# Performance work log

Measured on AMD Instinct MI355X. Metric: run time of the kernel, lower is better.

The kernel has to match this reference:

```python
import jax, jax.numpy as jnp
import numpy as np

N_LAYERS = 10


def _rel_graph_conv(x, src, dst, etype, W_rel, W_loop, b):
    # x: [N, h]; W_rel: [R, h, h] (per-relation weight), DGL low_mem style:
    # project all nodes by all relations, then gather per edge by (etype, src).
    xr = jnp.einsum('ni,rio->rno', x, W_rel)          # [R, N, h]
    m = xr[etype, src]                                 # [E, h] per-edge messages
    agg = jax.ops.segment_sum(m, dst, num_segments=x.shape[0])  # sum aggregation
    # DGL RelGraphConv defaults: self_loop=True, bias=True, no activation
    return agg + x @ W_loop + b


def setup_inputs() -> dict:
    key = jax.random.key(0)
    ks = jax.random.split(key, 12)
    N, E, F, H, R = 100000, 600000, 64, 128, 8
    inp = {
        'feats': jax.random.normal(ks[0], (N, F), dtype=jnp.float32),
        'src': jax.random.randint(ks[1], (E,), 0, N, dtype=jnp.int32),
        'dst': jax.random.randint(ks[2], (E,), 0, N, dtype=jnp.int32),
        'etype': jax.random.randint(ks[3], (E,), 0, R, dtype=jnp.int32),
    }
    s = 0.05
    inp['W_in'] = jax.random.normal(ks[4], (F, H), dtype=jnp.float32) * s
    inp['b_in'] = jnp.zeros((H,), dtype=jnp.float32)
    # stacked params for 10 layer-dependent GCNConv layers
    inp['W_rel'] = jax.random.normal(ks[5], (N_LAYERS, R, H, H), dtype=jnp.float32) * s
    inp['W_loop'] = jax.random.normal(ks[6], (N_LAYERS, H, H), dtype=jnp.float32) * s
    inp['b_rel'] = jnp.zeros((N_LAYERS, H), dtype=jnp.float32)
    inp['W_u1'] = jax.random.normal(ks[7], (N_LAYERS, 2 * H, 2 * H), dtype=jnp.float32) * s  # Linear(h+h, 2h)
    inp['b_u1'] = jnp.zeros((N_LAYERS, 2 * H), dtype=jnp.float32)
    inp['W_u2'] = jax.random.normal(ks[8], (N_LAYERS, 3 * H, H), dtype=jnp.float32) * s      # Linear(h+2h, h)
    inp['b_u2'] = jnp.zeros((N_LAYERS, H), dtype=jnp.float32)
    return inp


def reference(feats, src, dst, etype, W_in, b_in, W_rel, W_loop, b_rel, W_u1, b_u1, W_u2, b_u2):
    act = jnp.tanh  # activation_dict['tanh']
    x = act(feats @ W_in + b_in)  # conv_input
    for l in range(N_LAYERS):
        msg = _rel_graph_conv(x, src, dst, etype, W_rel[l], W_loop[l], b_rel[l])
        mid = act(jnp.concatenate([x, msg], axis=1) @ W_u1[l] + b_u1[l])
        out = jnp.concatenate([x, mid], axis=1) @ W_u2[l] + b_u2[l]
        x = act(out)
    return x
```

## Files before the change

kernel.cpp:

```cpp
#include <hip/hip_runtime.h>
#include <cstddef>


#define HID 128
#define NREL 8
#define NL 10

typedef __attribute__((ext_vector_type(8))) __bf16 bf16x8;
typedef __attribute__((ext_vector_type(4))) float f32x4;

__device__ __forceinline__ float fast_tanh(float x) {
  float cx = fminf(fmaxf(x, -10.f), 10.f);
  float z = exp2f(cx * 2.8853900817779268f);
  return (z - 1.f) * __builtin_amdgcn_rcpf(z + 1.f);
}

__global__ __launch_bounds__(256) void k_transpose(const float* __restrict__ W,
                                                   __bf16* __restrict__ Wt,
                                                   int K, int Nc,
                                                   int inDiv, int inScale, int inOff,
                                                   int outDiv, int outScale, int outOff) {
  __shared__ float t[32][33];
  int z = blockIdx.z;
  int zi = (z / inDiv) * inScale + (z % inDiv) + inOff;
  int zo = (z / outDiv) * outScale + (z % outDiv) + outOff;
  const float* Wz = W + (size_t)zi * K * Nc;
  __bf16* Wtz = Wt + (size_t)zo * K * Nc;
  int n0 = blockIdx.x * 32, k0 = blockIdx.y * 32;
#pragma unroll
  for (int i = 0; i < 4; i++) {
    int k = k0 + threadIdx.y + i * 8;
    int n = n0 + threadIdx.x;
    t[threadIdx.y + i * 8][threadIdx.x] = Wz[(size_t)k * Nc + n];
  }
  __syncthreads();
#pragma unroll
  for (int i = 0; i < 4; i++) {
    int n = n0 + threadIdx.y + i * 8;
    int k = k0 + threadIdx.x;
    Wtz[(size_t)n * K + k] = (__bf16)t[threadIdx.x][threadIdx.y + i * 8];
  }
}

__global__ __launch_bounds__(256) void k_fold_wu1(const float* __restrict__ Wu1,
                                                  const float* __restrict__ Wloop,
                                                  __bf16* __restrict__ wt) {
  int l = blockIdx.y;
  int n0 = blockIdx.x * 32;
  const float* wu1 = Wu1 + (size_t)l * 256 * 256;
  const float* wl = Wloop + (size_t)l * 128 * 128;
  __bf16* wtl = wt + (size_t)l * 256 * 256;
  __shared__ float bot[128][33];
  for (int t = threadIdx.x; t < 128 * 32; t += 256) {
    int j = t >> 5, c = t & 31;
    bot[j][c] = wu1[(size_t)(128 + j) * 256 + n0 + c];
  }
  __syncthreads();
  int k = threadIdx.x & 127;
  int half = threadIdx.x >> 7;
  float acc[16];
#pragma unroll
  for (int c = 0; c < 16; c++) acc[c] = 0.f;
  for (int j = 0; j < 128; j++) {
    float w = wl[(size_t)k * 128 + j];
#pragma unroll
    for (int c = 0; c < 16; c++) acc[c] += w * bot[j][half * 16 + c];
  }
#pragma unroll
  for (int c = 0; c < 16; c++) {
    int n = n0 + half * 16 + c;
    wtl[(size_t)n * 256 + k] = (__bf16)(wu1[(size_t)k * 256 + n] + acc[c]);
  }
}

__global__ __launch_bounds__(256) void k_cvt(const float* __restrict__ x,
                                             __bf16* __restrict__ y, int n4) {
  int i = blockIdx.x * 256 + threadIdx.x;
  if (i < n4) {
    float4 f = ((const float4*)x)[i];
    __bf16 o[4] = {(__bf16)f.x, (__bf16)f.y, (__bf16)f.z, (__bf16)f.w};
    *(uint2*)(y + (size_t)i * 4) = *(uint2*)o;
  }
}

__global__ __launch_bounds__(256) void k_zero(int* __restrict__ p, int n) {
  for (int i = blockIdx.x * 256 + threadIdx.x; i < n; i += gridDim.x * 256) p[i] = 0;
}

__global__ __launch_bounds__(256) void k_hist_row(const int* __restrict__ dst,
                                                  int E, int* __restrict__ rowCnt) {
  int e = blockIdx.x * 256 + threadIdx.x;
  if (e < E) atomicAdd(&rowCnt[dst[e]], 1);
}

__global__ __launch_bounds__(256) void k_scan_part(const int* __restrict__ rowCnt,
                                                   int nb, int* __restrict__ thrPre,
                                                   int* __restrict__ blkSum) {
  __shared__ int sdata[256];
  int tid = threadIdx.x;
  int gtid = blockIdx.x * 256 + tid;
  int tot = gridDim.x * 256;
  int chunk = (nb + tot - 1) / tot;
  int lo = gtid * chunk, hi = min(nb, lo + chunk);
  int s = 0;
  for (int i = lo; i < hi; i++) s += rowCnt[i];
  sdata[tid] = s;
  __syncthreads();
#pragma unroll
  for (int off = 1; off < 256; off <<= 1) {
    int t = (tid >= off) ? sdata[tid - off] : 0;
    __syncthreads();
    sdata[tid] += t;
    __syncthreads();
  }
  thrPre[gtid] = sdata[tid] - s;
  if (tid == 255) blkSum[blockIdx.x] = sdata[255];
}

__global__ __launch_bounds__(256) void k_scan_mid(const int* __restrict__ blkSum,
                                                  int nblk, int nb,
                                                  int* __restrict__ blkOff,
                                                  int* __restrict__ rowStart) {
  __shared__ int part[256];
  int tid = threadIdx.x;
  part[tid] = (tid < nblk) ? blkSum[tid] : 0;
  __syncthreads();
  if (tid == 0) {
    int a = 0;
    for (int i = 0; i < nblk; i++) { int v = part[i]; part[i] = a; a += v; }
    rowStart[nb] = a;
  }
  __syncthreads();
  if (tid < nblk) blkOff[tid] = part[tid];
}

__global__ __launch_bounds__(256) void k_scan_fin(const int* __restrict__ rowCnt,
                                                  int nb,
                                                  const int* __restrict__ thrPre,
                                                  const int* __restrict__ blkOff,
                                                  int* __restrict__ rowStart,
                                                  int* __restrict__ rowCur) {
  int tid = threadIdx.x;
  int gtid = blockIdx.x * 256 + tid;
  int tot = gridDim.x * 256;
  int chunk = (nb + tot - 1) / tot;
  int lo = gtid * chunk, hi = min(nb, lo + chunk);
  int run = blkOff[blockIdx.x] + thrPre[gtid];
  for (int i = lo; i < hi; i++) {
    rowStart[i] = run;
    rowCur[i] = run;
    run += rowCnt[i];
  }
}

__global__ __launch_bounds__(256) void k_place_row(const int* __restrict__ et,
                                                   const int* __restrict__ src,
                                                   const int* __restrict__ dst,
                                                   int* __restrict__ rowCur,
                                                   int* __restrict__ epk, int E) {
  int e = blockIdx.x * 256 + threadIdx.x;
  if (e < E) {
    int p = atomicAdd(&rowCur[dst[e]], 1);
    epk[p] = src[e] | (et[e] << 17);
  }
}

__global__ __launch_bounds__(256) void seg_sum(
    const __bf16* __restrict__ Z, const int* __restrict__ rowStart,
    const int* __restrict__ epk, const float* __restrict__ b_rel_l,
    __bf16* __restrict__ msgb, int N, int relBase, int zW) {
  int t16 = threadIdx.x & 15;
  int d = blockIdx.x * 16 + (threadIdx.x >> 4);
  if (d >= N) return;

  float acc[8];
  if (b_rel_l) {
#pragma unroll
    for (int z = 0; z < 8; z++) acc[z] = b_rel_l[t16 * 8 + z];
  } else {
    bf16x8 mv = *(const bf16x8*)(msgb + (size_t)d * HID + t16 * 8);
#pragma unroll
    for (int z = 0; z < 8; z++) acc[z] = (float)mv[z];
  }

  const int lo = rowStart[d], hi = rowStart[d + 1];
  for (int e0 = lo; e0 < hi; e0 += 4) {
    bf16x8 v[4];
    int take[4];
#pragma unroll
    for (int u = 0; u < 4; u++) {
      int e = e0 + u;
      int in = e < hi;
      int p = epk[in ? e : lo];
      int rr = (p >> 17) - relBase;
      int slot = rr & 3;
      v[u] = *(const bf16x8*)(Z + (size_t)(p & 0x1FFFF) * zW + slot * HID + t16 * 8);
      take[u] = in && ((unsigned)rr < 4u);
    }
#pragma unroll
    for (int u = 0; u < 4; u++) {
      if (take[u]) {
#pragma unroll
        for (int z = 0; z < 8; z++) acc[z] += (float)v[u][z];
      }
    }
  }

  bf16x8 o;
#pragma unroll
  for (int z = 0; z < 8; z++) o[z] = (__bf16)acc[z];
  *(bf16x8*)(msgb + (size_t)d * HID + t16 * 8) = o;
}

template <int K, int K0, int MINW>
__global__ __launch_bounds__(512, MINW) void gemm_lds(
    const __bf16* __restrict__ A0, const __bf16* __restrict__ A1,
    const __bf16* __restrict__ Bt, const float* __restrict__ bias,
    __bf16* __restrict__ Cb, float* __restrict__ Cf,
    int M, int Nc, int act) {
  constexpr int NS = K / 32;
  constexpr int NS0 = K0 / 32;
  constexpr int K1 = (K - K0) > 0 ? (K - K0) : 1;
  __shared__ __bf16 As[2][256][32];
  __shared__ __bf16 Bs[2][128][32];

  const int tid = threadIdx.x;

  int colt, mrow;
  {
    const int gx = gridDim.x;
    const int nb = gx * gridDim.y;
    const int id = blockIdx.x + blockIdx.y * gx;
    const int q = nb >> 3, r = nb & 7;
    const int xcd = id & 7, i = id >> 3;
    const int wk = (xcd < r) ? (xcd * (q + 1) + i)
                             : (r * (q + 1) + (xcd - r) * q + i);
    colt = wk % gx;
    mrow = wk / gx;
  }
  const int m0 = mrow * 256;
  const int bn0 = colt * 128;

  const int w = tid >> 6;
  const int lane = tid & 63;

  const int cA0 = w * 128 + lane;
  const int rA0 = cA0 >> 2, sA0 = cA0 & 3;
  const int cA1 = cA0 + 64;
  const int rA1 = cA1 >> 2, sA1 = cA1 & 3;
  const int cB = w * 64 + lane;
  const int rB = cB >> 2, sB = cB & 3;

  auto stage_step = [&](int b, int ks) {
    {
      const __bf16* g = Bt + (size_t)(bn0 + rB) * K + ks * 32 + sB * 8;
      __builtin_amdgcn_global_load_lds(
          (const __attribute__((address_space(1))) void*)g,
          (__attribute__((address_space(3))) void*)(&Bs[b][0][0] + (size_t)w * 512),
          16, 0, 0);
    }
    if (ks < NS0) {
      const __bf16* g0 = A0 + (size_t)(m0 + rA0) * K0 + ks * 32 + sA0 * 8;
      __builtin_amdgcn_global_load_lds(
          (const __attribute__((address_space(1))) void*)g0,
          (__attribute__((address_space(3))) void*)(&As[b][0][0] + (size_t)(w * 2 + 0) * 512),
          16, 0, 0);
      const __bf16* g1 = A0 + (size_t)(m0 + rA1) * K0 + ks * 32 + sA1 * 8;
      __builtin_amdgcn_global_load_lds(
          (const __attribute__((address_space(1))) void*)g1,
          (__attribute__((address_space(3))) void*)(&As[b][0][0] + (size_t)(w * 2 + 1) * 512),
          16, 0, 0);
    } else {
      const __bf16* g0 = A1 + (size_t)(m0 + rA0) * K1 + (ks - NS0) * 32 + sA0 * 8;
      __builtin_amdgcn_global_load_lds(
          (const __attribute__((address_space(1))) void*)g0,
          (__attribute__((address_space(3))) void*)(&As[b][0][0] + (size_t)(w * 2 + 0) * 512),
          16, 0, 0);
      const __bf16* g1 = A1 + (size_t)(m0 + rA1) * K1 + (ks - NS0) * 32 + sA1 * 8;
      __builtin_amdgcn_global_load_lds(
          (const __attribute__((address_space(1))) void*)g1,
          (__attribute__((address_space(3))) void*)(&As[b][0][0] + (size_t)(w * 2 + 1) * 512),
          16, 0, 0);
    }
  };

  const int ml = lane & 15, q2 = lane >> 4;
  const int wr = (w >> 1) * 64;
  const int wc = (w & 1) * 64;

  f32x4 acc[4][4];
#pragma unroll
  for (int i = 0; i < 4; i++)
#pragma unroll
    for (int j = 0; j < 4; j++)
#pragma unroll
      for (int r = 0; r < 4; r++) acc[i][j][r] = 0.f;

  stage_step(0, 0);
  if (NS > 1) stage_step(1, 1);

#pragma unroll
  for (int ks = 0; ks < NS; ks++) {
    const int cur = ks & 1;
    if (ks + 1 < NS) asm volatile("s_waitcnt vmcnt(3)" ::: "memory");
    else             asm volatile("s_waitcnt vmcnt(0)" ::: "memory");
    asm volatile("s_barrier" ::: "memory");

    bf16x8 af[4], bfr[4];
#pragma unroll
    for (int i = 0; i < 4; i++)
      af[i] = *(const bf16x8*)(&As[cur][wr + i * 16 + ml][q2 * 8]);
#pragma unroll
    for (int j = 0; j < 4; j++)
      bfr[j] = *(const bf16x8*)(&Bs[cur][wc + j * 16 + ml][q2 * 8]);
#pragma unroll
    for (int i = 0; i < 4; i++)
#pragma unroll
      for (int j = 0; j < 4; j++)
        acc[i][j] = __builtin_amdgcn_mfma_f32_16x16x32_bf16(af[i], bfr[j],
                                                            acc[i][j], 0, 0, 0);

    asm volatile("s_barrier" ::: "memory");
    if (ks + 2 < NS) stage_step(cur, ks + 2);
  }

#pragma unroll
  for (int i = 0; i < 4; i++) {
#pragma unroll
    for (int r = 0; r < 4; r++) {
      int grow = m0 + wr + i * 16 + q2 * 4 + r;
      if (grow >= M) continue;
#pragma unroll
      for (int j = 0; j < 4; j++) {
        int col = bn0 + wc + j * 16 + ml;
        float v = acc[i][j][r];
        if (bias) v += bias[col];
        if (act) v = fast_tanh(v);
        if (Cb) Cb[(size_t)grow * Nc + col] = (__bf16)v;
        if (Cf) Cf[(size_t)grow * Nc + col] = v;
      }
    }
  }
}

extern "C" void kernel_launch(void* const* d_in, const int* in_sizes, int n_in,
                              void* d_out, int out_size, void* d_ws, size_t ws_size,
                              hipStream_t stream) {
  const float* feats  = (const float*)d_in[0];
  const int*   src    = (const int*)d_in[1];
  const int*   dst    = (const int*)d_in[2];
  const int*   etype  = (const int*)d_in[3];
  const float* W_in   = (const float*)d_in[4];
  const float* b_in   = (const float*)d_in[5];
  const float* W_rel  = (const float*)d_in[6];
  const float* W_loop = (const float*)d_in[7];
  const float* b_rel  = (const float*)d_in[8];
  const float* W_u1   = (const float*)d_in[9];
  const float* b_u1   = (const float*)d_in[10];
  const float* W_u2   = (const float*)d_in[11];
  const float* b_u2   = (const float*)d_in[12];

  const int E = in_sizes[1];
  const int N = in_sizes[0] / 64;
  const int TS = HID * HID;

  __bf16* xb0  = (__bf16*)d_ws;
  __bf16* xb1  = xb0 + (size_t)N * HID;
  __bf16* msgb = xb1 + (size_t)N * HID;
  __bf16* U    = msgb + (size_t)N * HID;
  __bf16* Z    = U;
  __bf16* mid  = U;
  __bf16* featsb = U;
  __bf16* wt_in = U + (size_t)N * 640;
  __bf16* wt_z0 = wt_in + 128 * 64;
  __bf16* wt_z1 = wt_z0 + (size_t)10 * 4 * TS;
  __bf16* wt_u1 = wt_z1 + (size_t)10 * 4 * TS;
  __bf16* wt_u2 = wt_u1 + (size_t)10 * 256 * 256;
  int* rowCnt   = (int*)(wt_u2 + (size_t)10 * 128 * 384);
  int* rowStart = rowCnt + N;
  int* rowCur   = rowStart + N + 1;
  int* epk      = rowCur + N;
  int* thrPre   = epk + E;
  int* blkSum   = thrPre + 256 * 256;
  int* blkOff   = blkSum + 256;

  k_transpose<<<dim3(4, 2, 1), dim3(32, 8), 0, stream>>>(W_in, wt_in, 64, 128,
                                                         1, 1, 0, 1, 1, 0);
  k_transpose<<<dim3(4, 4, 40), dim3(32, 8), 0, stream>>>(W_rel, wt_z0, 128, 128,
                                                          4, 8, 0, 4, 4, 0);
  k_transpose<<<dim3(4, 4, 40), dim3(32, 8), 0, stream>>>(W_rel, wt_z1, 128, 128,
                                                          4, 8, 4, 4, 4, 0);
  k_transpose<<<dim3(8, 8, 10), dim3(32, 8), 0, stream>>>(W_u1, wt_u1, 256, 256,
                                                          1, 1, 0, 1, 1, 0);
  k_fold_wu1<<<dim3(8, 10), dim3(256), 0, stream>>>(W_u1, W_loop, wt_u1);
  k_transpose<<<dim3(4, 12, 10), dim3(32, 8), 0, stream>>>(W_u2, wt_u2, 384, 128,
                                                           1, 1, 0, 1, 1, 0);
  k_cvt<<<(N * 64 / 4 + 255) / 256, 256, 0, stream>>>(feats, featsb, N * 64 / 4);

  k_zero<<<128, 256, 0, stream>>>(rowCnt, N);
  k_hist_row<<<(E + 255) / 256, 256, 0, stream>>>(dst, E, rowCnt);
  k_scan_part<<<256, 256, 0, stream>>>(rowCnt, N, thrPre, blkSum);
  k_scan_mid<<<1, 256, 0, stream>>>(blkSum, 256, N, blkOff, rowStart);
  k_scan_fin<<<256, 256, 0, stream>>>(rowCnt, N, thrPre, blkOff, rowStart, rowCur);
  k_place_row<<<(E + 255) / 256, 256, 0, stream>>>(etype, src, dst, rowCur, epk, E);

  const dim3 blk(512);
  const int gm = (N + 255) / 256;
  const dim3 gseg((N + 15) / 16);

  gemm_lds<64, 64, 2><<<dim3(1, gm), blk, 0, stream>>>(
      featsb, featsb, wt_in, b_in, xb0, nullptr, N, HID, 1);

  for (int l = 0; l < NL; l++) {
    const __bf16* xin = (l & 1) ? xb1 : xb0;
    __bf16* xout = (l & 1) ? xb0 : xb1;

    gemm_lds<128, 128, 2><<<dim3(4, gm), blk, 0, stream>>>(
        xin, xin, wt_z0 + (size_t)l * 4 * TS, nullptr, Z, nullptr, N, 512, 0);
    seg_sum<<<gseg, dim3(256), 0, stream>>>(Z, rowStart, epk,
                                            b_rel + (size_t)l * HID,
                                            msgb, N, 0, 512);
    gemm_lds<128, 128, 2><<<dim3(4, gm), blk, 0, stream>>>(
        xin, xin, wt_z1 + (size_t)l * 4 * TS, nullptr, Z, nullptr, N, 512, 0);
    seg_sum<<<gseg, dim3(256), 0, stream>>>(Z, rowStart, epk, nullptr,
                                            msgb, N, 4, 512);

    gemm_lds<256, 128, 2><<<dim3(2, gm), blk, 0, stream>>>(
        xin, msgb, wt_u1 + (size_t)l * 256 * 256, b_u1 + (size_t)l * 256,
        mid, nullptr, N, 256, 1);

    gemm_lds<384, 128, 2><<<dim3(1, gm), blk, 0, stream>>>(
        xin, mid, wt_u2 + (size_t)l * HID * 384, b_u2 + (size_t)l * HID,
        (l == NL - 1) ? nullptr : xout,
        (l == NL - 1) ? (float*)d_out : nullptr,
        N, HID, 1);
  }
}
```

Measured before the change: 2.379 ms.

## Compute relation projections only for (relation, src) pairs used by edges

Builds per-relation flags and compacted index lists of source nodes that actually appear with each relation, then runs a gathered GEMM that projects only those rows into a compacted Z buffer. Edge records now store the compacted Z row instead of src/etype, and seg_sum reads from the compact layout. With about 600k edges over 800k (relation, node) pairs, roughly half the projection GEMM work is skipped. In exchange it adds one-time preprocessing kernels and gathered A-row loads, and the GEMM epilogue writes scalar bf16 values.

```diff
diff --git a/kernel.cpp b/kernel.cpp
--- a/kernel.cpp
+++ b/kernel.cpp
@@ -93,7 +93,26 @@
   if (e < E) atomicAdd(&rowCnt[dst[e]], 1);
 }
 
-__global__ __launch_bounds__(256) void k_scan_part(const int* __restrict__ rowCnt,
+__global__ __launch_bounds__(256) void k_flag(const int* __restrict__ et,
+                                              const int* __restrict__ src,
+                                              int E, int N,
+                                              int* __restrict__ F0,
+                                              int* __restrict__ F1) {
+  int e = blockIdx.x * 256 + threadIdx.x;
+  if (e < E) {
+    int r = et[e];
+    (r < 4 ? F0 : F1)[(r & 3) * N + src[e]] = 1;
+  }
+}
+
+__global__ __launch_bounds__(256) void k_srcof(const int* __restrict__ F,
+                                               const int* __restrict__ P,
+                                               int n, int N, int* __restrict__ srcOf) {
+  int i = blockIdx.x * 256 + threadIdx.x;
+  if (i < n && F[i]) srcOf[P[i]] = i % N;
+}
+
+__global__ __launch_bounds__(256) void k_scan_part(const int* __restrict__ cntArr,
                                                    int nb, int* __restrict__ thrPre,
                                                    int* __restrict__ blkSum) {
   __shared__ int sdata[256];
@@ -103,7 +122,7 @@
   int chunk = (nb + tot - 1) / tot;
   int lo = gtid * chunk, hi = min(nb, lo + chunk);
   int s = 0;
-  for (int i = lo; i < hi; i++) s += rowCnt[i];
+  for (int i = lo; i < hi; i++) s += cntArr[i];
   sdata[tid] = s;
   __syncthreads();
 #pragma unroll
@@ -120,7 +139,7 @@
 __global__ __launch_bounds__(256) void k_scan_mid(const int* __restrict__ blkSum,
                                                   int nblk, int nb,
                                                   int* __restrict__ blkOff,
-                                                  int* __restrict__ rowStart) {
+                                                  int* __restrict__ pre) {
   __shared__ int part[256];
   int tid = threadIdx.x;
   part[tid] = (tid < nblk) ? blkSum[tid] : 0;
@@ -128,18 +147,18 @@
   if (tid == 0) {
     int a = 0;
     for (int i = 0; i < nblk; i++) { int v = part[i]; part[i] = a; a += v; }
-    rowStart[nb] = a;
+    pre[nb] = a;
   }
   __syncthreads();
   if (tid < nblk) blkOff[tid] = part[tid];
 }
 
-__global__ __launch_bounds__(256) void k_scan_fin(const int* __restrict__ rowCnt,
+__global__ __launch_bounds__(256) void k_scan_fin(const int* __restrict__ cntArr,
                                                   int nb,
                                                   const int* __restrict__ thrPre,
                                                   const int* __restrict__ blkOff,
-                                                  int* __restrict__ rowStart,
-                                                  int* __restrict__ rowCur) {
+                                                  int* __restrict__ pre,
+                                                  int* __restrict__ cur) {
   int tid = threadIdx.x;
   int gtid = blockIdx.x * 256 + tid;
   int tot = gridDim.x * 256;
@@ -147,28 +166,34 @@
   int lo = gtid * chunk, hi = min(nb, lo + chunk);
   int run = blkOff[blockIdx.x] + thrPre[gtid];
   for (int i = lo; i < hi; i++) {
-    rowStart[i] = run;
-    rowCur[i] = run;
-    run += rowCnt[i];
+    pre[i] = run;
+    if (cur) cur[i] = run;
+    run += cntArr[i];
   }
 }
 
 __global__ __launch_bounds__(256) void k_place_row(const int* __restrict__ et,
                                                    const int* __restrict__ src,
                                                    const int* __restrict__ dst,
+                                                   const int* __restrict__ P0,
+                                                   const int* __restrict__ P1,
                                                    int* __restrict__ rowCur,
-                                                   int* __restrict__ epk, int E) {
+                                                   int* __restrict__ epk, int E, int N) {
   int e = blockIdx.x * 256 + threadIdx.x;
   if (e < E) {
     int p = atomicAdd(&rowCur[dst[e]], 1);
-    epk[p] = src[e] | (et[e] << 17);
+    int r = et[e];
+    int half = r >> 2;
+    const int* P = half ? P1 : P0;
+    int zrow = P[(r & 3) * N + src[e]];
+    epk[p] = zrow | (half << 19);
   }
 }
 
 __global__ __launch_bounds__(256) void seg_sum(
-    const __bf16* __restrict__ Z, const int* __restrict__ rowStart,
+    const __bf16* __restrict__ Zc, const int* __restrict__ rowStart,
     const int* __restrict__ epk, const float* __restrict__ b_rel_l,
-    __bf16* __restrict__ msgb, int N, int relBase, int zW) {
+    __bf16* __restrict__ msgb, int N, int half) {
   int t16 = threadIdx.x & 15;
   int d = blockIdx.x * 16 + (threadIdx.x >> 4);
   if (d >= N) return;
@@ -192,10 +217,9 @@
       int e = e0 + u;
       int in = e < hi;
       int p = epk[in ? e : lo];
-      int rr = (p >> 17) - relBase;
-      int slot = rr & 3;
-      v[u] = *(const bf16x8*)(Z + (size_t)(p & 0x1FFFF) * zW + slot * HID + t16 * 8);
-      take[u] = in && ((unsigned)rr < 4u);
+      int zrow = p & 0x7FFFF;
+      v[u] = *(const bf16x8*)(Zc + (size_t)zrow * HID + t16 * 8);
+      take[u] = in && ((p >> 19) == half);
     }
 #pragma unroll
     for (int u = 0; u < 4; u++) {
@@ -210,6 +234,118 @@
 #pragma unroll
   for (int z = 0; z < 8; z++) o[z] = (__bf16)acc[z];
   *(bf16x8*)(msgb + (size_t)d * HID + t16 * 8) = o;
+}
+
+__global__ __launch_bounds__(512, 2) void gemm_gather(
+    const __bf16* __restrict__ X, const __bf16* __restrict__ Wt4,
+    const int* __restrict__ srcOf, const int* __restrict__ Pf,
+    __bf16* __restrict__ Zc, int N) {
+  constexpr int K = 128, NS = 4;
+  __shared__ __bf16 As[2][256][32];
+  __shared__ __bf16 Bs[2][128][32];
+
+  const int tid = threadIdx.x;
+  int colt, mrow;
+  {
+    const int gx = gridDim.x;
+    const int nb = gx * gridDim.y;
+    const int id = blockIdx.x + blockIdx.y * gx;
+    const int q = nb >> 3, r8 = nb & 7;
+    const int xcd = id & 7, i = id >> 3;
+    const int wk = (xcd < r8) ? (xcd * (q + 1) + i)
+                              : (r8 * (q + 1) + (xcd - r8) * q + i);
+    colt = wk % gx;
+    mrow = wk / gx;
+  }
+  const int rel = colt;
+  const int base = Pf[rel * N];
+  const int nxt = Pf[(rel + 1) * N];
+  const int cnt = nxt - base;
+  const int m0 = mrow * 256;
+  if (m0 >= cnt) return;
+  const __bf16* Bt = Wt4 + (size_t)rel * K * 128;
+
+  const int w = tid >> 6, lane = tid & 63;
+  const int cA0 = w * 128 + lane;
+  const int rA0 = cA0 >> 2, sA0 = cA0 & 3;
+  const int cA1 = cA0 + 64;
+  const int rA1 = cA1 >> 2, sA1 = cA1 & 3;
+  const int cB = w * 64 + lane;
+  const int rB = cB >> 2, sB = cB & 3;
+
+  const int src0 = srcOf[min(base + m0 + rA0, nxt - 1)];
+  const int src1 = srcOf[min(base + m0 + rA1, nxt - 1)];
+  const __bf16* a0 = X + (size_t)src0 * K + sA0 * 8;
+  const __bf16* a1 = X + (size_t)src1 * K + sA1 * 8;
+
+  auto stage_step = [&](int b, int ks) {
+    const __bf16* g = Bt + (size_t)rB * K + ks * 32 + sB * 8;
+    __builtin_amdgcn_global_load_lds(
+        (const __attribute__((address_space(1))) void*)g,
+        (__attribute__((address_space(3))) void*)(&Bs[b][0][0] + (size_t)w * 512),
+        16, 0, 0);
+    __builtin_amdgcn_global_load_lds(
+        (const __attribute__((address_space(1))) void*)(a0 + ks * 32),
+        (__attribute__((address_space(3))) void*)(&As[b][0][0] + (size_t)(w * 2 + 0) * 512),
+        16, 0, 0);
+    __builtin_amdgcn_global_load_lds(
+        (const __attribute__((address_space(1))) void*)(a1 + ks * 32),
+        (__attribute__((address_space(3))) void*)(&As[b][0][0] + (size_t)(w * 2 + 1) * 512),
+        16, 0, 0);
+  };
+
+  const int ml = lane & 15, q2 = lane >> 4;
+  const int wr = (w >> 1) * 64, wc = (w & 1) * 64;
+
+  f32x4 acc[4][4];
+#pragma unroll
+  for (int i = 0; i < 4; i++)
+#pragma unroll
+    for (int j = 0; j < 4; j++)
+#pragma unroll
+      for (int r = 0; r < 4; r++) acc[i][j][r] = 0.f;
+
+  stage_step(0, 0);
+  stage_step(1, 1);
+
+#pragma unroll
+  for (int ks = 0; ks < NS; ks++) {
+    const int cur = ks & 1;
+    if (ks + 1 < NS) asm volatile("s_waitcnt vmcnt(3)" ::: "memory");
+    else             asm volatile("s_waitcnt vmcnt(0)" ::: "memory");
+    asm volatile("s_barrier" ::: "memory");
+
+    bf16x8 af[4], bfr[4];
+#pragma unroll
+    for (int i = 0; i < 4; i++)
+      af[i] = *(const bf16x8*)(&As[cur][wr + i * 16 + ml][q2 * 8]);
+#pragma unroll
+    for (int j = 0; j < 4; j++)
+      bfr[j] = *(const bf16x8*)(&Bs[cur][wc + j * 16 + ml][q2 * 8]);
+#pragma unroll
+    for (int i = 0; i < 4; i++)
+#pragma unroll
+      for (int j = 0; j < 4; j++)
+        acc[i][j] = __builtin_amdgcn_mfma_f32_16x16x32_bf16(af[i], bfr[j],
+                                                            acc[i][j], 0, 0, 0);
+
+    asm volatile("s_barrier" ::: "memory");
+    if (ks + 2 < NS) stage_step(cur, ks + 2);
+  }
+
+#pragma unroll
+  for (int i = 0; i < 4; i++) {
+#pragma unroll
+    for (int r = 0; r < 4; r++) {
+      int lrow = m0 + wr + i * 16 + q2 * 4 + r;
+      if (lrow >= cnt) continue;
+#pragma unroll
+      for (int j = 0; j < 4; j++) {
+        int col = wc + j * 16 + ml;
+        Zc[(size_t)(base + lrow) * HID + col] = (__bf16)acc[i][j][r];
+      }
+    }
+  }
 }
 
 template <int K, int K0, int MINW>
@@ -225,16 +361,15 @@
   __shared__ __bf16 Bs[2][128][32];
 
   const int tid = threadIdx.x;
-
   int colt, mrow;
   {
     const int gx = gridDim.x;
     const int nb = gx * gridDim.y;
     const int id = blockIdx.x + blockIdx.y * gx;
-    const int q = nb >> 3, r = nb & 7;
+    const int q = nb >> 3, r8 = nb & 7;
     const int xcd = id & 7, i = id >> 3;
-    const int wk = (xcd < r) ? (xcd * (q + 1) + i)
-                             : (r * (q + 1) + (xcd - r) * q + i);
+    const int wk = (xcd < r8) ? (xcd * (q + 1) + i)
+                              : (r8 * (q + 1) + (xcd - r8) * q + i);
     colt = wk % gx;
     mrow = wk / gx;
   }
@@ -383,6 +518,12 @@
   int* thrPre   = epk + E;
   int* blkSum   = thrPre + 256 * 256;
   int* blkOff   = blkSum + 256;
+  int* F0       = blkOff + 256;
+  int* F1       = F0 + 4 * N;
+  int* P0       = F1 + 4 * N;
+  int* P1       = P0 + 4 * N + 1;
+  int* S0       = P1 + 4 * N + 1;
+  int* S1       = S0 + 4 * N;
 
   k_transpose<<<dim3(4, 2, 1), dim3(32, 8), 0, stream>>>(W_in, wt_in, 64, 128,
                                                          1, 1, 0, 1, 1, 0);
@@ -398,11 +539,23 @@
   k_cvt<<<(N * 64 / 4 + 255) / 256, 256, 0, stream>>>(feats, featsb, N * 64 / 4);
 
   k_zero<<<128, 256, 0, stream>>>(rowCnt, N);
+  k_zero<<<256, 256, 0, stream>>>(F0, 4 * N);
+  k_zero<<<256, 256, 0, stream>>>(F1, 4 * N);
   k_hist_row<<<(E + 255) / 256, 256, 0, stream>>>(dst, E, rowCnt);
+  k_flag<<<(E + 255) / 256, 256, 0, stream>>>(etype, src, E, N, F0, F1);
   k_scan_part<<<256, 256, 0, stream>>>(rowCnt, N, thrPre, blkSum);
   k_scan_mid<<<1, 256, 0, stream>>>(blkSum, 256, N, blkOff, rowStart);
   k_scan_fin<<<256, 256, 0, stream>>>(rowCnt, N, thrPre, blkOff, rowStart, rowCur);
-  k_place_row<<<(E + 255) / 256, 256, 0, stream>>>(etype, src, dst, rowCur, epk, E);
+  k_scan_part<<<256, 256, 0, stream>>>(F0, 4 * N, thrPre, blkSum);
+  k_scan_mid<<<1, 256, 0, stream>>>(blkSum, 256, 4 * N, blkOff, P0);
+  k_scan_fin<<<256, 256, 0, stream>>>(F0, 4 * N, thrPre, blkOff, P0, nullptr);
+  k_scan_part<<<256, 256, 0, stream>>>(F1, 4 * N, thrPre, blkSum);
+  k_scan_mid<<<1, 256, 0, stream>>>(blkSum, 256, 4 * N, blkOff, P1);
+  k_scan_fin<<<256, 256, 0, stream>>>(F1, 4 * N, thrPre, blkOff, P1, nullptr);
+  k_srcof<<<(4 * N + 255) / 256, 256, 0, stream>>>(F0, P0, 4 * N, N, S0);
+  k_srcof<<<(4 * N + 255) / 256, 256, 0, stream>>>(F1, P1, 4 * N, N, S1);
+  k_place_row<<<(E + 255) / 256, 256, 0, stream>>>(etype, src, dst, P0, P1,
+                                                   rowCur, epk, E, N);
 
   const dim3 blk(512);
   const int gm = (N + 255) / 256;
@@ -415,15 +568,15 @@
     const __bf16* xin = (l & 1) ? xb1 : xb0;
     __bf16* xout = (l & 1) ? xb0 : xb1;
 
-    gemm_lds<128, 128, 2><<<dim3(4, gm), blk, 0, stream>>>(
-        xin, xin, wt_z0 + (size_t)l * 4 * TS, nullptr, Z, nullptr, N, 512, 0);
+    gemm_gather<<<dim3(4, gm), blk, 0, stream>>>(
+        xin, wt_z0 + (size_t)l * 4 * TS, S0, P0, Z, N);
     seg_sum<<<gseg, dim3(256), 0, stream>>>(Z, rowStart, epk,
                                             b_rel + (size_t)l * HID,
-                                            msgb, N, 0, 512);
-    gemm_lds<128, 128, 2><<<dim3(4, gm), blk, 0, stream>>>(
-        xin, xin, wt_z1 + (size_t)l * 4 * TS, nullptr, Z, nullptr, N, 512, 0);
+                                            msgb, N, 0);
+    gemm_gather<<<dim3(4, gm), blk, 0, stream>>>(
+        xin, wt_z1 + (size_t)l * 4 * TS, S1, P1, Z, N);
     seg_sum<<<gseg, dim3(256), 0, stream>>>(Z, rowStart, epk, nullptr,
-                                            msgb, N, 4, 512);
+                                            msgb, N, 1);
 
     gemm_lds<256, 128, 2><<<dim3(2, gm), blk, 0, stream>>>(
         xin, msgb, wt_u1 + (size_t)l * 256 * 256, b_u1 + (size_t)l * 256,
```

Result: faster. 2.294 ms (-3.6%).
